# Performance work log

Measured on AMD Instinct MI355X. Metric: run time of the kernel, lower is better.

## Reference

```python
import jax, jax.numpy as jnp
import numpy as np
from jax.ops import segment_sum

HIDDEN = 128  # hard-coded in VGAEModel.__init__


def gcn_conv(x, W, b, src, dst, n_nodes):
    """PyG GCNConv: h = x@W; add self-loops; symmetric norm D^-1/2 A D^-1/2; scatter-add; +bias."""
    h = x @ W  # [N, out]
    loop = jnp.arange(n_nodes, dtype=src.dtype)
    s = jnp.concatenate([src, loop])  # [E+N]
    d = jnp.concatenate([dst, loop])  # [E+N]
    deg = segment_sum(jnp.ones_like(d, dtype=h.dtype), d, num_segments=n_nodes)  # [N]
    dinv = jnp.where(deg > 0, jax.lax.rsqrt(deg), 0.0)
    norm = dinv[s] * dinv[d]  # [E+N]
    msg = h[s] * norm[:, None]  # [E+N, out] -- largest intermediate
    out = segment_sum(msg, d, num_segments=n_nodes)  # [N, out]
    return out + b


def setup_inputs() -> dict:
    key = jax.random.key(0)
    ks = jax.random.split(key, 8)
    N, E, IN, OUT = 50000, 1600000, 256, 64
    x = jax.random.normal(ks[0], (N, IN), dtype=jnp.float32)
    edge_index = jax.random.randint(ks[1], (2, E), 0, N, dtype=jnp.int32)
    sc = lambda fan_in: 1.0 / np.sqrt(fan_in)
    W1 = jax.random.uniform(ks[2], (IN, HIDDEN), jnp.float32, -sc(IN), sc(IN))
    b1 = jnp.zeros((HIDDEN,), jnp.float32)
    W_mu = jax.random.uniform(ks[3], (HIDDEN, OUT), jnp.float32, -sc(HIDDEN), sc(HIDDEN))
    b_mu = jnp.zeros((OUT,), jnp.float32)
    W_ls = jax.random.uniform(ks[4], (HIDDEN, OUT), jnp.float32, -sc(HIDDEN), sc(HIDDEN))
    b_ls = jnp.zeros((OUT,), jnp.float32)
    return {"x": x, "edge_index": edge_index, "n_nodes": N,
            "W1": W1, "b1": b1, "W_mu": W_mu, "b_mu": b_mu, "W_ls": W_ls, "b_ls": b_ls}


def reference(x, edge_index, n_nodes, W1, b1, W_mu, b_mu, W_ls, b_ls):
    src, dst = edge_index[0], edge_index[1]
    h = jax.nn.relu(gcn_conv(x, W1, b1, src, dst, n_nodes))
    mu = gcn_conv(h, W_mu, b_mu, src, dst, n_nodes)
    logstd = gcn_conv(h, W_ls, b_ls, src, dst, n_nodes)
    return (mu, logstd)
```

## Files before the change

### kernel.cpp

```cpp
#include <hip/hip_runtime.h>
#include <hip/hip_fp16.h>


#define IN_DIM 256
#define F1 128
#define F2 64
#define QF 32
#define BN 128
#define CAP 4736
#define BIN_EDGES 4096
#define SIDW 1024
#define SBLK 512

typedef _Float16 f16x8 __attribute__((ext_vector_type(8)));
typedef _Float16 f16x4 __attribute__((ext_vector_type(4)));
typedef float f32x4 __attribute__((ext_vector_type(4)));

static inline int cdiv_i(int a, int b) { return (a + b - 1) / b; }

__device__ static inline uint32_t lds_addr(const void* p) {
    return (uint32_t)(size_t)(const __attribute__((address_space(3))) void*)p;
}

__global__ void k_prep_frags(const float* __restrict__ W1,
                             const float* __restrict__ Wmu,
                             const float* __restrict__ Wls,
                             __half* __restrict__ W1frag,
                             __half* __restrict__ Wcfrag) {
    int t = blockIdx.x * blockDim.x + threadIdx.x;
    if (t < 8 * 8 * 64) {
        int lane = t & 63, nt = (t >> 6) & 7, ks = t >> 9;
        int k0 = ks * 32 + ((lane >> 4) << 3);
        int n = nt * 16 + (lane & 15);
#pragma unroll
        for (int j = 0; j < 8; ++j)
            W1frag[(size_t)t * 8 + j] = __float2half(W1[(k0 + j) * F1 + n]);
    } else if (t < 8 * 8 * 64 + 4 * 8 * 64) {
        int u = t - 8 * 8 * 64;
        int lane = u & 63, nt = (u >> 6) & 7, ks = u >> 9;
        int k0 = ks * 32 + ((lane >> 4) << 3);
        int c = nt * 16 + (lane & 15);
        const float* W = (c < F2) ? (Wmu + c) : (Wls + (c - F2));
#pragma unroll
        for (int j = 0; j < 8; ++j)
            Wcfrag[(size_t)u * 8 + j] = __float2half(W[(k0 + j) * F2]);
    }
}

__global__ __launch_bounds__(512) void k_binning(const int* __restrict__ src,
                                                 const int* __restrict__ dst,
                                                 int* __restrict__ bcur,
                                                 int* __restrict__ pairs, int E) {
    __shared__ int hcnt[512];
    __shared__ int hrank[512];
    __shared__ int hbase[512];
    __shared__ int lbase[512];
    __shared__ int stage[BIN_EDGES];
    __shared__ int gaddr[BIN_EDGES];
    const int tid = threadIdx.x;
    hcnt[tid] = 0; hrank[tid] = 0;
    __syncthreads();
    const int e0 = blockIdx.x * BIN_EDGES;
    int s_[8], d_[8];
#pragma unroll
    for (int it = 0; it < 8; ++it) {
        int e = e0 + it * 512 + tid;
        if (e < E) {
            s_[it] = src[e];
            d_[it] = dst[e];
            atomicAdd(&hcnt[d_[it] >> 7], 1);
        } else {
            d_[it] = -1;
        }
    }
    __syncthreads();
    int v = hcnt[tid];
    lbase[tid] = v;
    __syncthreads();
    for (int ofs = 1; ofs < 512; ofs <<= 1) {
        int add = (tid >= ofs) ? lbase[tid - ofs] : 0;
        __syncthreads();
        lbase[tid] += add;
        __syncthreads();
    }
    int total = lbase[511];
    int excl = lbase[tid] - v;
    __syncthreads();
    lbase[tid] = excl;
    hbase[tid] = v ? atomicAdd(&bcur[tid], v) : 0;
    __syncthreads();
#pragma unroll
    for (int it = 0; it < 8; ++it) {
        if (d_[it] >= 0) {
            int b = d_[it] >> 7;
            int r = atomicAdd(&hrank[b], 1);
            int li = lbase[b] + r;
            stage[li] = ((d_[it] & (BN - 1)) << 16) | s_[it];
            gaddr[li] = b * CAP + hbase[b] + r;
        }
    }
    __syncthreads();
    for (int i = tid; i < total; i += 512)
        pairs[gaddr[i]] = stage[i];
}

__global__ __launch_bounds__(512) void k_bucket_build(const int* __restrict__ pairs,
                                                      const int* __restrict__ bcur,
                                                      float* __restrict__ dinv,
                                                      int* __restrict__ rs,
                                                      int* __restrict__ re,
                                                      ushort* __restrict__ ssrc, int N) {
    __shared__ int hist[BN];
    __shared__ int offs[BN];
    __shared__ int stage[CAP];
    const int b = blockIdx.x;
    const int n0 = b * BN;
    const int tid = threadIdx.x;
    const int pbase = b * CAP;
    const int cnt = min(bcur[b], CAP);
    if (tid < BN) hist[tid] = 0;
    __syncthreads();
    for (int e = tid; e < cnt; e += 512)
        atomicAdd(&hist[pairs[pbase + e] >> 16], 1);
    __syncthreads();
    if (tid < BN) offs[tid] = hist[tid];
    __syncthreads();
    for (int ofs = 1; ofs < BN; ofs <<= 1) {
        int add = 0;
        if (tid < BN && tid >= ofs) add = offs[tid - ofs];
        __syncthreads();
        if (tid < BN) offs[tid] += add;
        __syncthreads();
    }
    if (tid < BN) {
        int incl = offs[tid];
        int excl = incl - hist[tid];
        int n = n0 + tid;
        if (n < N) {
            dinv[n] = rsqrtf((float)hist[tid] + 1.0f);
            rs[n] = pbase + excl;
            re[n] = pbase + incl;
        }
        offs[tid] = excl;
    }
    __syncthreads();
    for (int e = tid; e < cnt; e += 512) {
        int p = pairs[pbase + e];
        int idx = atomicAdd(&offs[p >> 16], 1);
        stage[idx] = p & 0xFFFF;
    }
    __syncthreads();
    for (int i = tid; i < cnt; i += 512)
        ssrc[pbase + i] = (ushort)stage[i];
}

__global__ __launch_bounds__(256) void k_gemm1_mfma(const float* __restrict__ x,
                                                    const __half* __restrict__ W1frag,
                                                    const float* __restrict__ dinv,
                                                    __half* __restrict__ C, int M) {
    const int wave = threadIdx.x >> 6;
    const int lane = threadIdx.x & 63;
    const int m0 = blockIdx.x * 64 + wave * 16;
    if (m0 >= M) return;
    const int q = lane >> 4;
    const int arow = m0 + (lane & 15);
    f32x4 acc[8] = {};
#pragma unroll
    for (int ks = 0; ks < 8; ++ks) {
        const float* ap = x + (size_t)arow * IN_DIM + ks * 32 + q * 8;
        f32x4 f0 = *(const f32x4*)(ap);
        f32x4 f1 = *(const f32x4*)(ap + 4);
        f16x8 a = { (_Float16)f0.x, (_Float16)f0.y, (_Float16)f0.z, (_Float16)f0.w,
                    (_Float16)f1.x, (_Float16)f1.y, (_Float16)f1.z, (_Float16)f1.w };
        const __half* bbase = W1frag + ((size_t)(ks * 8) * 64 + lane) * 8;
#pragma unroll
        for (int nt = 0; nt < 8; ++nt) {
            f16x8 bfrag = *(const f16x8*)(bbase + (size_t)nt * 64 * 8);
            acc[nt] = __builtin_amdgcn_mfma_f32_16x16x32_f16(a, bfrag, acc[nt], 0, 0, 0);
        }
    }
    float dv[4];
#pragma unroll
    for (int r = 0; r < 4; ++r) dv[r] = dinv[m0 + q * 4 + r];
#pragma unroll
    for (int nt = 0; nt < 8; ++nt) {
        int col = nt * 16 + (lane & 15);
        __half* cq = C + (size_t)(col >> 5) * M * QF + (col & 31);
#pragma unroll
        for (int r = 0; r < 4; ++r)
            cq[(size_t)(m0 + q * 4 + r) * QF] = __float2half(acc[nt][r] * dv[r]);
    }
}

__global__ __launch_bounds__(256) void k_gemm2_mfma(const __half* __restrict__ A,
                                                    const __half* __restrict__ Wcfrag,
                                                    const float* __restrict__ dinv,
                                                    __half* __restrict__ C, int M) {
    const int wave = threadIdx.x >> 6;
    const int lane = threadIdx.x & 63;
    const int m0 = blockIdx.x * 64 + wave * 16;
    if (m0 >= M) return;
    const int q = lane >> 4;
    const int arow = m0 + (lane & 15);
    f32x4 acc[8] = {};
#pragma unroll
    for (int ks = 0; ks < 4; ++ks) {
        f16x8 a = *(const f16x8*)(A + (size_t)ks * M * QF + (size_t)arow * QF + q * 8);
        const __half* bbase = Wcfrag + ((size_t)(ks * 8) * 64 + lane) * 8;
#pragma unroll
        for (int nt = 0; nt < 8; ++nt) {
            f16x8 bfrag = *(const f16x8*)(bbase + (size_t)nt * 64 * 8);
            acc[nt] = __builtin_amdgcn_mfma_f32_16x16x32_f16(a, bfrag, acc[nt], 0, 0, 0);
        }
    }
    float dv[4];
#pragma unroll
    for (int r = 0; r < 4; ++r) dv[r] = dinv[m0 + q * 4 + r];
#pragma unroll
    for (int nt = 0; nt < 8; ++nt) {
        int col = nt * 16 + (lane & 15);
        __half* cq = C + (size_t)(col >> 5) * M * QF + (col & 31);
#pragma unroll
        for (int r = 0; r < 4; ++r)
            cq[(size_t)(m0 + q * 4 + r) * QF] = __float2half(acc[nt][r] * dv[r]);
    }
}

#define GLDS(GP, LP)                                                           \
    __builtin_amdgcn_global_load_lds(                                          \
        (const __attribute__((address_space(1))) void*)(GP),                   \
        (__attribute__((address_space(3))) void*)(LP), 16, 0, 0)

#define BODY(C_, C0, C1, C2, C3, N0, N1, N2, N3, SIA, SIB, SOA, SOB)           \
    {                                                                          \
        asm volatile("s_waitcnt lgkmcnt(4)" ::: "memory");                     \
        __builtin_amdgcn_sched_barrier(0);                                     \
        const __half* gA_ = tq + (size_t)(SIA) * QF + b8;                      \
        const __half* gB_ = tq + (size_t)(SIB) * QF + b8;                      \
        __half* LB_ = stg + ((((C_) + 3) & 3) << 10);                          \
        GLDS(gA_, LB_);                                                        \
        GLDS(gB_, LB_ + 512);                                                  \
        asm volatile("s_waitcnt vmcnt(4)" ::: "memory");                       \
        const uint32_t sva_ = sbb + 2u * (uint32_t)min(                        \
            ofs + ((C_) + 4) * 32 + e4, SIDW - 17);                            \
        const uint32_t tra_ = vaBase + ((uint32_t)(((C_) + 1) & 3) << 11);     \
        asm volatile(                                                          \
            "ds_read_u16 %0, %6\n\t"                                           \
            "ds_read_u16 %1, %6 offset:32\n\t"                                 \
            "ds_read_b64_tr_b16 %2, %7 offset:0\n\t"                           \
            "ds_read_b64_tr_b16 %3, %7 offset:1024\n\t"                        \
            "ds_read_b64_tr_b16 %4, %7 offset:32\n\t"                          \
            "ds_read_b64_tr_b16 %5, %7 offset:1056"                            \
            : "=&v"(SOA), "=&v"(SOB), "=&v"(N0), "=&v"(N1), "=&v"(N2),         \
              "=&v"(N3)                                                        \
            : "v"(sva_), "v"(tra_) : "memory");                                \
        const int eb_ = ebase + (C_) * 32;                                     \
        f16x8 af_;                                                             \
        _Pragma("unroll")                                                      \
        for (int j = 0; j < 8; ++j) {                                          \
            int m_ = eb_ + (j & 3) + ((j >> 2) << 4);                          \
            af_[j] = ((unsigned)m_ < dd) ? (_Float16)1.0f : (_Float16)0.0f;    \
        }                                                                      \
        asm volatile("s_waitcnt lgkmcnt(6)" ::: "memory");                     \
        __builtin_amdgcn_sched_barrier(0);                                     \
        f16x8 bf0_, bf1_;                                                      \
        _Pragma("unroll")                                                      \
        for (int j = 0; j < 4; ++j) {                                          \
            bf0_[j] = (C0)[j]; bf0_[j + 4] = (C1)[j];                          \
            bf1_[j] = (C2)[j]; bf1_[j + 4] = (C3)[j];                          \
        }                                                                      \
        acc0 = __builtin_amdgcn_mfma_f32_16x16x32_f16(af_, bf0_, acc0, 0, 0, 0); \
        acc1 = __builtin_amdgcn_mfma_f32_16x16x32_f16(af_, bf1_, acc1, 0, 0, 0); \
    }

template<bool FIRST>
__global__ __launch_bounds__(256) void k_gather_mfma(
        const int* __restrict__ rs, const int* __restrict__ re,
        const ushort* __restrict__ ssrc, const float* __restrict__ dinv,
        const __half* __restrict__ t,
        const float* __restrict__ bA, const float* __restrict__ bB,
        __half* __restrict__ h, float* __restrict__ out,
        int N, int NG) {
    __shared__ __align__(16) __half  smem[4][4][1024];
    __shared__ __align__(16) ushort  sidx[4][SIDW];
    const int wave = threadIdx.x >> 6;
    const int lane = threadIdx.x & 63;
    const int x = blockIdx.x & 7;
    const int q = x >> 1;
    const int g = (((blockIdx.x >> 3) << 1) + (x & 1)) * 4 + wave;
    if (g >= NG) return;
    const int nb = g << 4;
    const int e4 = lane >> 2;
    const int b8 = (lane & 3) * 8;
    const int col = lane & 15;
    const __half* tq = t + (size_t)q * N * QF;
    __half* stg = &smem[wave][0][0];
    ushort* sb = &sidx[wave][0];
    const uint32_t sbb = lds_addr(sb);
    const int o0 = rs[nb + col];
    const int o1 = re[nb + col];
    const int gs = rs[nb];
    const int ge = re[nb + 15];
    const int ne = ge - gs;
    const int nc = (ne + 31) >> 5;
    const int m0 = (lane >> 4) << 2;
    const int ebase = gs + m0 - o0;
    const unsigned dd = (unsigned)(o1 - o0);
    const uint32_t voff = 256u * (uint32_t)(lane >> 4)
                        + 64u * (uint32_t)((lane >> 2) & 3)
                        + 8u * (uint32_t)(lane & 3);
    const uint32_t vaBase = lds_addr(stg) + voff;
    f32x4 acc0 = {}, acc1 = {};

    const int gsa = gs & ~7;
    const int ofs = gs - gsa;

    if (nc > 0) {
        const int nblk = min((ofs + ne + SBLK - 1) / SBLK, SIDW / SBLK);
        for (int b = 0; b < nblk; ++b)
            GLDS(ssrc + gsa + b * SBLK + lane * 8, sb + b * SBLK);
        asm volatile("s_waitcnt vmcnt(0)" ::: "memory");
#pragma unroll
        for (int p = 0; p < 3; ++p) {
            const int ia = min(ofs + p * 32 + e4, SIDW - 17);
            const int sA = sb[ia], sB = sb[ia + 16];
            __half* LB = stg + (p << 10);
            GLDS(tq + (size_t)sA * QF + b8, LB);
            GLDS(tq + (size_t)sB * QF + b8, LB + 512);
        }
        uint32_t sv1A, sv1B, sv2A, sv2B;
        f16x4 RA0, RA1, RA2, RA3, RB0, RB1, RB2, RB3;
        {
            const uint32_t sva_ = sbb + 2u * (uint32_t)min(ofs + 96 + e4, SIDW - 17);
            asm volatile(
                "ds_read_u16 %0, %6\n\t"
                "ds_read_u16 %1, %6 offset:32\n\t"
                "ds_read_b64_tr_b16 %2, %7 offset:0\n\t"
                "ds_read_b64_tr_b16 %3, %7 offset:1024\n\t"
                "ds_read_b64_tr_b16 %4, %7 offset:32\n\t"
                "ds_read_b64_tr_b16 %5, %7 offset:1056"
                : "=&v"(sv1A), "=&v"(sv1B), "=&v"(RA0), "=&v"(RA1),
                  "=&v"(RA2), "=&v"(RA3)
                : "v"(sva_), "v"(vaBase) : "memory");
        }
        int c = 0;
        for (; c + 1 < nc; c += 2) {
            BODY(c,     RA0, RA1, RA2, RA3, RB0, RB1, RB2, RB3,
                 sv1A, sv1B, sv2A, sv2B);
            BODY(c + 1, RB0, RB1, RB2, RB3, RA0, RA1, RA2, RA3,
                 sv2A, sv2B, sv1A, sv1B);
        }
        if (c < nc) {
            asm volatile("s_waitcnt lgkmcnt(0)" ::: "memory");
            __builtin_amdgcn_sched_barrier(0);
            const int eb_ = ebase + c * 32;
            f16x8 af_;
#pragma unroll
            for (int j = 0; j < 8; ++j) {
                int m_ = eb_ + (j & 3) + ((j >> 2) << 4);
                af_[j] = ((unsigned)m_ < dd) ? (_Float16)1.0f : (_Float16)0.0f;
            }
            f16x8 bf0_, bf1_;
#pragma unroll
            for (int j = 0; j < 4; ++j) {
                bf0_[j] = RA0[j]; bf0_[j + 4] = RA1[j];
                bf1_[j] = RA2[j]; bf1_[j + 4] = RA3[j];
            }
            acc0 = __builtin_amdgcn_mfma_f32_16x16x32_f16(af_, bf0_, acc0, 0, 0, 0);
            acc1 = __builtin_amdgcn_mfma_f32_16x16x32_f16(af_, bf1_, acc1, 0, 0, 0);
        }
        asm volatile("s_waitcnt vmcnt(0)" ::: "memory");
    }
    const int nl0 = (lane >> 4) << 2;
#pragma unroll
    for (int r2 = 0; r2 < 4; ++r2) {
        const int node = nb + nl0 + r2;
        const float di = dinv[node];
        const float s0 = __half2float(tq[(size_t)node * QF + col]);
        const float s1 = __half2float(tq[(size_t)node * QF + 16 + col]);
        float v0 = (acc0[r2] + s0) * di;
        float v1 = (acc1[r2] + s1) * di;
        if constexpr (FIRST) {
            v0 += bA[q * QF + col];
            v1 += bA[q * QF + 16 + col];
            _Float16* hp = (_Float16*)(h + (size_t)q * N * QF + (size_t)node * QF);
            __builtin_nontemporal_store((_Float16)fmaxf(v0, 0.f), hp + col);
            __builtin_nontemporal_store((_Float16)fmaxf(v1, 0.f), hp + 16 + col);
        } else {
            const float* bp = (q < 2) ? bA : bB;
            const int fb = (q & 1) * QF;
            v0 += bp[fb + col];
            v1 += bp[fb + 16 + col];
            float* op = (q < 2) ? (out + (size_t)node * F2 + fb)
                                : (out + (size_t)N * F2 + (size_t)node * F2 + fb);
            __builtin_nontemporal_store(v0, op + col);
            __builtin_nontemporal_store(v1, op + 16 + col);
        }
    }
}

extern "C" void kernel_launch(void* const* d_in, const int* in_sizes, int n_in,
                              void* d_out, int out_size, void* d_ws, size_t ws_size,
                              hipStream_t stream) {
    const float* x   = (const float*)d_in[0];
    const int*   ei  = (const int*)d_in[1];
    const float* W1  = (const float*)d_in[3];
    const float* b1  = (const float*)d_in[4];
    const float* Wmu = (const float*)d_in[5];
    const float* bmu = (const float*)d_in[6];
    const float* Wls = (const float*)d_in[7];
    const float* bls = (const float*)d_in[8];

    const int N = in_sizes[0] / IN_DIM;
    const int E = in_sizes[1] / 2;
    const int* src = ei;
    const int* dst = ei + E;
    float* out = (float*)d_out;
    const int nbuck = cdiv_i(N, BN);

    size_t off = 0;
    auto carve = [&](size_t n) { size_t o = off; off += (n + 3) & ~(size_t)3; return o; };
    float* ws = (float*)d_ws;
    float*  dinv   =        ws + carve(N);
    int*    rs     = (int*)(ws + carve(N));
    int*    re     = (int*)(ws + carve(N));
    int*    bcur   = (int*)(ws + carve(512));
    ushort* ssrc   = (ushort*)(ws + carve(((size_t)nbuck * CAP + 2048) / 2));
    __half* t16    = (__half*)(ws + carve((size_t)N * F1 / 2));
    __half* h16    = (__half*)(ws + carve((size_t)N * F1 / 2));
    __half* W1frag = (__half*)(ws + carve(8 * 8 * 64 * 8 / 2));
    __half* Wcfrag = (__half*)(ws + carve(4 * 8 * 64 * 8 / 2));
    (void)ws_size;
    int* pairs = (int*)t16;
    __half* t2_16 = t16;

    k_prep_frags<<<cdiv_i(8 * 8 * 64 + 4 * 8 * 64, 256), 256, 0, stream>>>(
        W1, Wmu, Wls, W1frag, Wcfrag);

    hipMemsetAsync(bcur, 0, sizeof(int) * 512, stream);
    k_binning<<<cdiv_i(E, BIN_EDGES), 512, 0, stream>>>(src, dst, bcur, pairs, E);
    k_bucket_build<<<nbuck, 512, 0, stream>>>(pairs, bcur, dinv, rs, re, ssrc, N);

    const int NG = N >> 4;
    const int NBI = cdiv_i(NG, 8);

    k_gemm1_mfma<<<cdiv_i(N, 64), 256, 0, stream>>>(x, W1frag, dinv, t16, N);
    k_gather_mfma<true><<<8 * NBI, 256, 0, stream>>>(
        rs, re, ssrc, dinv, t16, b1, b1, h16, out, N, NG);
    k_gemm2_mfma<<<cdiv_i(N, 64), 256, 0, stream>>>(h16, Wcfrag, dinv, t2_16, N);
    k_gather_mfma<false><<<8 * NBI, 256, 0, stream>>>(
        rs, re, ssrc, dinv, t2_16, bmu, bls, h16, out, N, NG);
}
```

Baseline: 239.6 us.

## Replace bucketed two-pass CSR build with global histogram, scan, atomic scatter

Replaces the LDS-staged bucket binning and per-bucket sort with a plain CSR build: a global atomic histogram of destinations, a two-level prefix scan, a finalize kernel that writes row offsets and dinv, and an atomic-cursor scatter of source indices. This removes the fixed-capacity per-bucket layout, including the CAP clamp that could drop edges, and the intermediate pairs buffer. In exchange it uses heavy global atomics, and the scatter writes are unordered within each row, so neighbor order becomes nondeterministic. It also adds more kernel launches.

```diff
diff --git a/kernel.cpp b/kernel.cpp
--- a/kernel.cpp
+++ b/kernel.cpp
@@ -6,9 +6,6 @@
 #define F1 128
 #define F2 64
 #define QF 32
-#define BN 128
-#define CAP 4736
-#define BIN_EDGES 4096
 #define SIDW 1024
 #define SBLK 512
 
@@ -47,111 +44,79 @@
     }
 }
 
-__global__ __launch_bounds__(512) void k_binning(const int* __restrict__ src,
+__global__ __launch_bounds__(512) void k_hist(const int* __restrict__ dst,
+                                              int* __restrict__ cnt, int E) {
+    const int e0 = blockIdx.x * 4096 + threadIdx.x;
+#pragma unroll
+    for (int i = 0; i < 8; ++i) {
+        int e = e0 + i * 512;
+        if (e < E) atomicAdd(&cnt[dst[e]], 1);
+    }
+}
+
+__global__ __launch_bounds__(1024) void k_scan1(const int* __restrict__ cnt,
+                                                int* __restrict__ rs,
+                                                int* __restrict__ bsum, int N) {
+    __shared__ int s[1024];
+    const int t = threadIdx.x;
+    const int n = blockIdx.x * 1024 + t;
+    int v = (n < N) ? cnt[n] : 0;
+    s[t] = v;
+    __syncthreads();
+    for (int o = 1; o < 1024; o <<= 1) {
+        int a = (t >= o) ? s[t - o] : 0;
+        __syncthreads();
+        s[t] += a;
+        __syncthreads();
+    }
+    if (n < N) rs[n] = s[t] - v;
+    if (t == 1023) bsum[blockIdx.x] = s[1023];
+}
+
+__global__ __launch_bounds__(64) void k_scan2(int* __restrict__ bsum, int nb) {
+    __shared__ int s[64];
+    const int t = threadIdx.x;
+    int v = (t < nb) ? bsum[t] : 0;
+    s[t] = v;
+    __syncthreads();
+    for (int o = 1; o < 64; o <<= 1) {
+        int a = (t >= o) ? s[t - o] : 0;
+        __syncthreads();
+        s[t] += a;
+        __syncthreads();
+    }
+    if (t < nb) bsum[t] = s[t] - v;
+}
+
+__global__ __launch_bounds__(1024) void k_fin(const int* __restrict__ cnt,
+                                              const int* __restrict__ bsum,
+                                              int* __restrict__ rs,
+                                              int* __restrict__ re,
+                                              int* __restrict__ cur,
+                                              float* __restrict__ dinv, int N) {
+    const int n = blockIdx.x * 1024 + threadIdx.x;
+    if (n >= N) return;
+    const int base = rs[n] + bsum[blockIdx.x];
+    const int c = cnt[n];
+    rs[n] = base;
+    re[n] = base + c;
+    cur[n] = base;
+    dinv[n] = rsqrtf((float)c + 1.0f);
+}
+
+__global__ __launch_bounds__(512) void k_scatter(const int* __restrict__ src,
                                                  const int* __restrict__ dst,
-                                                 int* __restrict__ bcur,
-                                                 int* __restrict__ pairs, int E) {
-    __shared__ int hcnt[512];
-    __shared__ int hrank[512];
-    __shared__ int hbase[512];
-    __shared__ int lbase[512];
-    __shared__ int stage[BIN_EDGES];
-    __shared__ int gaddr[BIN_EDGES];
-    const int tid = threadIdx.x;
-    hcnt[tid] = 0; hrank[tid] = 0;
-    __syncthreads();
-    const int e0 = blockIdx.x * BIN_EDGES;
-    int s_[8], d_[8];
-#pragma unroll
-    for (int it = 0; it < 8; ++it) {
-        int e = e0 + it * 512 + tid;
+                                                 int* __restrict__ cur,
+                                                 ushort* __restrict__ ssrc, int E) {
+    const int e0 = blockIdx.x * 4096 + threadIdx.x;
+#pragma unroll
+    for (int i = 0; i < 8; ++i) {
+        int e = e0 + i * 512;
         if (e < E) {
-            s_[it] = src[e];
-            d_[it] = dst[e];
-            atomicAdd(&hcnt[d_[it] >> 7], 1);
-        } else {
-            d_[it] = -1;
-        }
-    }
-    __syncthreads();
-    int v = hcnt[tid];
-    lbase[tid] = v;
-    __syncthreads();
-    for (int ofs = 1; ofs < 512; ofs <<= 1) {
-        int add = (tid >= ofs) ? lbase[tid - ofs] : 0;
-        __syncthreads();
-        lbase[tid] += add;
-        __syncthreads();
-    }
-    int total = lbase[511];
-    int excl = lbase[tid] - v;
-    __syncthreads();
-    lbase[tid] = excl;
-    hbase[tid] = v ? atomicAdd(&bcur[tid], v) : 0;
-    __syncthreads();
-#pragma unroll
-    for (int it = 0; it < 8; ++it) {
-        if (d_[it] >= 0) {
-            int b = d_[it] >> 7;
-            int r = atomicAdd(&hrank[b], 1);
-            int li = lbase[b] + r;
-            stage[li] = ((d_[it] & (BN - 1)) << 16) | s_[it];
-            gaddr[li] = b * CAP + hbase[b] + r;
-        }
-    }
-    __syncthreads();
-    for (int i = tid; i < total; i += 512)
-        pairs[gaddr[i]] = stage[i];
-}
-
-__global__ __launch_bounds__(512) void k_bucket_build(const int* __restrict__ pairs,
-                                                      const int* __restrict__ bcur,
-                                                      float* __restrict__ dinv,
-                                                      int* __restrict__ rs,
-                                                      int* __restrict__ re,
-                                                      ushort* __restrict__ ssrc, int N) {
-    __shared__ int hist[BN];
-    __shared__ int offs[BN];
-    __shared__ int stage[CAP];
-    const int b = blockIdx.x;
-    const int n0 = b * BN;
-    const int tid = threadIdx.x;
-    const int pbase = b * CAP;
-    const int cnt = min(bcur[b], CAP);
-    if (tid < BN) hist[tid] = 0;
-    __syncthreads();
-    for (int e = tid; e < cnt; e += 512)
-        atomicAdd(&hist[pairs[pbase + e] >> 16], 1);
-    __syncthreads();
-    if (tid < BN) offs[tid] = hist[tid];
-    __syncthreads();
-    for (int ofs = 1; ofs < BN; ofs <<= 1) {
-        int add = 0;
-        if (tid < BN && tid >= ofs) add = offs[tid - ofs];
-        __syncthreads();
-        if (tid < BN) offs[tid] += add;
-        __syncthreads();
-    }
-    if (tid < BN) {
-        int incl = offs[tid];
-        int excl = incl - hist[tid];
-        int n = n0 + tid;
-        if (n < N) {
-            dinv[n] = rsqrtf((float)hist[tid] + 1.0f);
-            rs[n] = pbase + excl;
-            re[n] = pbase + incl;
-        }
-        offs[tid] = excl;
-    }
-    __syncthreads();
-    for (int e = tid; e < cnt; e += 512) {
-        int p = pairs[pbase + e];
-        int idx = atomicAdd(&offs[p >> 16], 1);
-        stage[idx] = p & 0xFFFF;
-    }
-    __syncthreads();
-    for (int i = tid; i < cnt; i += 512)
-        ssrc[pbase + i] = (ushort)stage[i];
+            int p = atomicAdd(&cur[dst[e]], 1);
+            ssrc[p] = (ushort)src[e];
+        }
+    }
 }
 
 __global__ __launch_bounds__(256) void k_gemm1_mfma(const float* __restrict__ x,
@@ -416,7 +381,6 @@
     const int* src = ei;
     const int* dst = ei + E;
     float* out = (float*)d_out;
-    const int nbuck = cdiv_i(N, BN);
 
     size_t off = 0;
     auto carve = [&](size_t n) { size_t o = off; off += (n + 3) & ~(size_t)3; return o; };
@@ -424,22 +388,27 @@
     float*  dinv   =        ws + carve(N);
     int*    rs     = (int*)(ws + carve(N));
     int*    re     = (int*)(ws + carve(N));
-    int*    bcur   = (int*)(ws + carve(512));
-    ushort* ssrc   = (ushort*)(ws + carve(((size_t)nbuck * CAP + 2048) / 2));
+    int*    cnt    = (int*)(ws + carve(N));
+    int*    cur    = (int*)(ws + carve(N));
+    int*    bsum   = (int*)(ws + carve(64));
+    ushort* ssrc   = (ushort*)(ws + carve(((size_t)E + 1024) / 2 + 4));
     __half* t16    = (__half*)(ws + carve((size_t)N * F1 / 2));
     __half* h16    = (__half*)(ws + carve((size_t)N * F1 / 2));
     __half* W1frag = (__half*)(ws + carve(8 * 8 * 64 * 8 / 2));
     __half* Wcfrag = (__half*)(ws + carve(4 * 8 * 64 * 8 / 2));
     (void)ws_size;
-    int* pairs = (int*)t16;
     __half* t2_16 = t16;
 
     k_prep_frags<<<cdiv_i(8 * 8 * 64 + 4 * 8 * 64, 256), 256, 0, stream>>>(
         W1, Wmu, Wls, W1frag, Wcfrag);
 
-    hipMemsetAsync(bcur, 0, sizeof(int) * 512, stream);
-    k_binning<<<cdiv_i(E, BIN_EDGES), 512, 0, stream>>>(src, dst, bcur, pairs, E);
-    k_bucket_build<<<nbuck, 512, 0, stream>>>(pairs, bcur, dinv, rs, re, ssrc, N);
+    const int NT = cdiv_i(N, 1024);
+    hipMemsetAsync(cnt, 0, sizeof(int) * N, stream);
+    k_hist<<<cdiv_i(E, 4096), 512, 0, stream>>>(dst, cnt, E);
+    k_scan1<<<NT, 1024, 0, stream>>>(cnt, rs, bsum, N);
+    k_scan2<<<1, 64, 0, stream>>>(bsum, NT);
+    k_fin<<<NT, 1024, 0, stream>>>(cnt, bsum, rs, re, cur, dinv, N);
+    k_scatter<<<cdiv_i(E, 4096), 512, 0, stream>>>(src, dst, cur, ssrc, E);
 
     const int NG = N >> 4;
     const int NBI = cdiv_i(NG, 8);
```

Measured after the change: 447.5 us. 86.8% more time.
